# Kernel optimization log

Measured on AMD Instinct MI355X. Metric: run time of the kernel, lower is better.

## Reference

```python
import jax, jax.numpy as jnp
import numpy as np

N_NODES = 50000
N_EDGES = 600000
CLASSIC_DIM = 128
GRAPH_OUTPUT_DIM = 96
NUM_RELATIONS = 4


def setup_inputs() -> dict:
    key = jax.random.key(0)
    ks = jax.random.split(key, 10)
    x = jax.random.normal(ks[0], (N_NODES, CLASSIC_DIM), dtype=jnp.float32)
    edge_index = jax.random.randint(ks[1], (2, N_EDGES), 0, N_NODES, dtype=jnp.int64)
    edge_type = jax.random.randint(ks[2], (N_EDGES,), 0, NUM_RELATIONS, dtype=jnp.int64)
    s1 = 1.0 / np.sqrt(CLASSIC_DIM)
    W_root1 = jax.random.normal(ks[3], (CLASSIC_DIM, CLASSIC_DIM), dtype=jnp.float32) * s1
    W_rel1 = jax.random.normal(ks[4], (NUM_RELATIONS, CLASSIC_DIM, CLASSIC_DIM), dtype=jnp.float32) * s1
    b1 = jnp.zeros((CLASSIC_DIM,), dtype=jnp.float32)
    W_root2 = jax.random.normal(ks[5], (CLASSIC_DIM, GRAPH_OUTPUT_DIM), dtype=jnp.float32) * s1
    W_rel2 = jax.random.normal(ks[6], (NUM_RELATIONS, CLASSIC_DIM, GRAPH_OUTPUT_DIM), dtype=jnp.float32) * s1
    b2 = jnp.zeros((GRAPH_OUTPUT_DIM,), dtype=jnp.float32)
    return {"classic_features": x, "edge_index": edge_index, "edge_type": edge_type,
            "W_root1": W_root1, "W_rel1": W_rel1, "b1": b1,
            "W_root2": W_root2, "W_rel2": W_rel2, "b2": b2}


def _rgcn_layer(x, edge_index, edge_type, W_root, W_rel, b):
    # RGCN: h_i = W_root x_i + b + sum_r (1/deg_{i,r}) * W_r * sum_{j in N_r(i)} x_j
    # Aggregate-then-transform (valid by linearity) to keep the matmul small.
    src, dst = edge_index[0], edge_index[1]
    msgs = x[src]  # [E, d_in] irregular gather
    out = x @ W_root + b
    n = x.shape[0]
    num_rel = W_rel.shape[0]
    for r in range(num_rel):  # small fixed loop over relation types
        mask = (edge_type == r).astype(x.dtype)  # [E]
        agg = jax.ops.segment_sum(msgs * mask[:, None], dst, num_segments=n)  # [N, d_in]
        deg = jax.ops.segment_sum(mask, dst, num_segments=n)  # [N]
        agg = agg / jnp.maximum(deg, 1.0)[:, None]  # mean per relation (PyG default norm)
        out = out + agg @ W_rel[r]
    return out


def reference(classic_features, edge_index, edge_type, W_root1, W_rel1, b1, W_root2, W_rel2, b2):
    h = _rgcn_layer(classic_features, edge_index, edge_type, W_root1, W_rel1, b1)
    h = jax.nn.relu(h)
    # dropout(0.2) is identity in eval mode
    out = _rgcn_layer(h, edge_index, edge_type, W_root2, W_rel2, b2)
    return out
```

## Files before the change

kernel.cpp:

```cpp
#include <hip/hip_runtime.h>

#define DIM_IN 128
#define NREL 4
#define KTOT (DIM_IN + NREL * DIM_IN)
#define CAP 32

typedef __attribute__((ext_vector_type(8))) short short8;
typedef __attribute__((ext_vector_type(4))) float floatx4;

__device__ inline unsigned short f2bf(float f) {
    union { float f; unsigned int i; } c;
    c.f = f;
    unsigned int r = c.i + 0x7FFF + ((c.i >> 16) & 1);
    return (unsigned short)(r >> 16);
}
__device__ inline float bf2f(unsigned short u) {
    union { unsigned int i; float f; } c;
    c.i = ((unsigned int)u) << 16;
    return c.f;
}

__device__ inline void gload16_lds(const void* g, void* l) {
    __builtin_amdgcn_global_load_lds((const __attribute__((address_space(1))) unsigned int*)g,
                                     (__attribute__((address_space(3))) unsigned int*)l,
                                     16, 0, 0);
}

__global__ __launch_bounds__(256) void prep_kernel(
    const float* __restrict__ x, unsigned short* __restrict__ xb, int n4,
    const float* __restrict__ Wroot1, const float* __restrict__ Wrel1,
    unsigned short* __restrict__ Wt1,
    const float* __restrict__ Wroot2, const float* __restrict__ Wrel2,
    unsigned short* __restrict__ Wt2,
    const int* __restrict__ ei, const int* __restrict__ et,
    int* __restrict__ counts, unsigned short* __restrict__ bucket, int E) {
    int t = blockIdx.x * 256 + threadIdx.x;
    if (t < E) {
        int b = ei[E + t] * NREL + et[t];
        int slot = atomicAdd(&counts[b], 1);
        if (slot < CAP) bucket[(size_t)b * CAP + slot] = (unsigned short)ei[t];
    }
    if (t < n4) {
        float4 v = ((const float4*)x)[t];
        ushort4 o;
        o.x = f2bf(v.x); o.y = f2bf(v.y); o.z = f2bf(v.z); o.w = f2bf(v.w);
        ((ushort4*)xb)[t] = o;
    }
    if (t < 128 * KTOT) {
        int n = t / KTOT, k = t - n * KTOT;
        float v = (k < DIM_IN) ? Wroot1[(size_t)k * 128 + n]
                               : Wrel1[(size_t)(k - DIM_IN) * 128 + n];
        Wt1[t] = f2bf(v);
    }
    if (t < 96 * KTOT) {
        int n = t / KTOT, k = t - n * KTOT;
        float v = (k < DIM_IN) ? Wroot2[(size_t)k * 96 + n]
                               : Wrel2[(size_t)(k - DIM_IN) * 96 + n];
        Wt2[t] = f2bf(v);
    }
}

__global__ __launch_bounds__(256) void agg_kernel(
    const unsigned short* __restrict__ feat, const unsigned short* __restrict__ bucket,
    const int* __restrict__ counts, unsigned short* __restrict__ agg, int nb) {
    int l16 = threadIdx.x & 15;
    int g = (blockIdx.x * 256 + threadIdx.x) >> 4;
    if (g >= nb) return;
    int cnt = counts[g];
    int m = (cnt < CAP) ? cnt : CAP;
    const unsigned short* bk = bucket + (size_t)g * CAP;
    const unsigned short* fb = feat + l16 * 8;
    float acc[8];
#pragma unroll
    for (int j = 0; j < 8; j++) acc[j] = 0.f;
    for (int base = 0; base < m; base += 16) {
        int mm = m - base;
        if (mm > 16) mm = 16;
        int pick = (l16 < mm) ? l16 : (mm - 1);
        int idx = bk[base + pick];
        int s0 = __shfl(idx, 0, 16);
        short8 u = *(const short8*)(fb + (size_t)s0 * DIM_IN);
        for (int j = 1; j < mm; j++) {
            int sn = __shfl(idx, j, 16);
            short8 un = *(const short8*)(fb + (size_t)sn * DIM_IN);
#pragma unroll
            for (int c = 0; c < 8; c++) acc[c] += bf2f((unsigned short)u[c]);
            u = un;
        }
#pragma unroll
        for (int c = 0; c < 8; c++) acc[c] += bf2f((unsigned short)u[c]);
    }
    float sc = (cnt > 0) ? (1.0f / (float)cnt) : 0.f;
    short8 o;
#pragma unroll
    for (int j = 0; j < 8; j++) o[j] = (short)f2bf(acc[j] * sc);
    *(short8*)(agg + (size_t)g * DIM_IN + l16 * 8) = o;
}

template <int NOUT, bool STORE_BF16_RELU>
__global__ __launch_bounds__(256) void mfma_gemm_kernel(
    const unsigned short* __restrict__ xb,
    const unsigned short* __restrict__ agg,
    const unsigned short* __restrict__ Wt,
    const float* __restrict__ bias,
    void* __restrict__ outp,
    int N) {
    constexpr int NT = NOUT / 32;
    constexpr int APAN = 64 * 32;
    constexpr int BPAN = NOUT * 32;
    __shared__ unsigned short sA[2 * APAN];
    __shared__ unsigned short sB[2 * BPAN];
    const int t = threadIdx.x;
    const int w = t >> 6;
    const int lane = t & 63;
    const int q = lane >> 4;
    const int l15 = lane & 15;
    const int wm = w >> 1, wn = w & 1;
    const int m0 = blockIdx.x * 64;

    floatx4 acc[2][NT];
#pragma unroll
    for (int mt = 0; mt < 2; mt++)
#pragma unroll
        for (int nt = 0; nt < NT; nt++) acc[mt][nt] = (floatx4)0.f;

    for (int ks = 0; ks < KTOT / 64; ks++) {
        const int k0 = ks * 64;
#pragma unroll
        for (int r = 0; r < 2; r++) {
            int idx = t + r * 256;
            int panel = idx >> 8;
            int rem = idx & 255;
            int row = rem >> 2, ch = rem & 3;
            int rowg = m0 + row;
            if (rowg >= N) rowg = N - 1;
            int col = panel * 32 + ch * 8;
            const unsigned short* gp =
                (k0 < DIM_IN)
                    ? (xb + (size_t)rowg * DIM_IN + k0 + col)
                    : (agg + (size_t)rowg * (NREL * DIM_IN) + (k0 - DIM_IN) + col);
            gload16_lds(gp, sA + (size_t)idx * 8);
        }
#pragma unroll
        for (int r = 0; r < (NOUT * 8) / 256; r++) {
            int idx = t + r * 256;
            int panel = idx / (NOUT * 4);
            int rem = idx - panel * (NOUT * 4);
            int nrow = rem >> 2, ch = rem & 3;
            gload16_lds(Wt + (size_t)nrow * KTOT + k0 + panel * 32 + ch * 8,
                        sB + (size_t)idx * 8);
        }
        __syncthreads();
#pragma unroll
        for (int s = 0; s < 2; s++) {
            short8 aF[2], bF[NT];
#pragma unroll
            for (int mt = 0; mt < 2; mt++)
                aF[mt] = *(const short8*)(sA + s * APAN +
                                          (size_t)(wm * 32 + mt * 16 + l15) * 32 + q * 8);
#pragma unroll
            for (int nt = 0; nt < NT; nt++)
                bF[nt] = *(const short8*)(sB + s * BPAN +
                                          (size_t)(wn * (NOUT / 2) + nt * 16 + l15) * 32 + q * 8);
#pragma unroll
            for (int mt = 0; mt < 2; mt++)
#pragma unroll
                for (int nt = 0; nt < NT; nt++)
                    acc[mt][nt] = __builtin_amdgcn_mfma_f32_16x16x32_bf16(aF[mt], bF[nt],
                                                                          acc[mt][nt], 0, 0, 0);
        }
        __syncthreads();
    }

#pragma unroll
    for (int nt = 0; nt < NT; nt++) {
        int colg = wn * (NOUT / 2) + nt * 16 + l15;
        float bv = bias[colg];
#pragma unroll
        for (int mt = 0; mt < 2; mt++) {
            int rbase = m0 + wm * 32 + mt * 16 + q * 4;
#pragma unroll
            for (int r = 0; r < 4; r++) {
                int grow = rbase + r;
                if (grow < N) {
                    float v = acc[mt][nt][r] + bv;
                    if (STORE_BF16_RELU) {
                        v = fmaxf(v, 0.f);
                        ((unsigned short*)outp)[(size_t)grow * NOUT + colg] = f2bf(v);
                    } else {
                        ((float*)outp)[(size_t)grow * NOUT + colg] = v;
                    }
                }
            }
        }
    }
}

extern "C" void kernel_launch(void* const* d_in, const int* in_sizes, int n_in,
                              void* d_out, int out_size, void* d_ws, size_t ws_size,
                              hipStream_t stream) {
    const float* x = (const float*)d_in[0];
    const int* ei = (const int*)d_in[1];
    const int* et = (const int*)d_in[2];
    const float* Wroot1 = (const float*)d_in[3];
    const float* Wrel1 = (const float*)d_in[4];
    const float* b1 = (const float*)d_in[5];
    const float* Wroot2 = (const float*)d_in[6];
    const float* Wrel2 = (const float*)d_in[7];
    const float* b2 = (const float*)d_in[8];
    float* out = (float*)d_out;

    int N = in_sizes[0] / DIM_IN;
    int E = in_sizes[2];
    int nb = N * NREL;

    char* p = (char*)d_ws;
    unsigned short* xb = (unsigned short*)p;     p += (size_t)N * DIM_IN * 2;
    unsigned short* hb = (unsigned short*)p;     p += (size_t)N * DIM_IN * 2;
    unsigned short* agg = (unsigned short*)p;    p += (size_t)nb * DIM_IN * 2;
    unsigned short* Wt1 = (unsigned short*)p;    p += (size_t)128 * KTOT * 2;
    unsigned short* Wt2 = (unsigned short*)p;    p += (size_t)96 * KTOT * 2;
    int* counts = (int*)p;                       p += (size_t)nb * 4;
    unsigned short* bucket = (unsigned short*)p; p += (size_t)nb * CAP * 2;
    if ((size_t)(p - (char*)d_ws) > ws_size) return;

    int n4 = N * DIM_IN / 4;
    int prepWork = n4;
    if (prepWork < E) prepWork = E;
    if (prepWork < 128 * KTOT) prepWork = 128 * KTOT;

    hipMemsetAsync(counts, 0, (size_t)nb * sizeof(int), stream);
    prep_kernel<<<(prepWork + 255) / 256, 256, 0, stream>>>(
        x, xb, n4, Wroot1, Wrel1, Wt1, Wroot2, Wrel2, Wt2, ei, et, counts, bucket, E);

    int gAgg = (nb * 16 + 255) / 256;
    int gB = (N + 63) / 64;
    agg_kernel<<<gAgg, 256, 0, stream>>>(xb, bucket, counts, agg, nb);
    mfma_gemm_kernel<128, true><<<gB, 256, 0, stream>>>(xb, agg, Wt1, b1, hb, N);
    agg_kernel<<<gAgg, 256, 0, stream>>>(hb, bucket, counts, agg, nb);
    mfma_gemm_kernel<96, false><<<gB, 256, 0, stream>>>(hb, agg, Wt2, b2, out, N);
}
```

Baseline: 228.3 us.

## Fuse all stages into one persistent cooperative kernel with grid syncs

```diff
diff --git a/kernel.cpp b/kernel.cpp
--- a/kernel.cpp
+++ b/kernel.cpp
@@ -1,4 +1,7 @@
 #include <hip/hip_runtime.h>
+#include <hip/hip_cooperative_groups.h>
+
+namespace cg = cooperative_groups;
 
 #define DIM_IN 128
 #define NREL 4
@@ -26,15 +29,15 @@
                                      16, 0, 0);
 }
 
-__global__ __launch_bounds__(256) void prep_kernel(
-    const float* __restrict__ x, unsigned short* __restrict__ xb, int n4,
+
+__device__ __forceinline__ void prep_body(
+    int t, const float* __restrict__ x, unsigned short* __restrict__ xb, int n4,
     const float* __restrict__ Wroot1, const float* __restrict__ Wrel1,
     unsigned short* __restrict__ Wt1,
     const float* __restrict__ Wroot2, const float* __restrict__ Wrel2,
     unsigned short* __restrict__ Wt2,
     const int* __restrict__ ei, const int* __restrict__ et,
     int* __restrict__ counts, unsigned short* __restrict__ bucket, int E) {
-    int t = blockIdx.x * 256 + threadIdx.x;
     if (t < E) {
         int b = ei[E + t] * NREL + et[t];
         int slot = atomicAdd(&counts[b], 1);
@@ -60,12 +63,10 @@
     }
 }
 
-__global__ __launch_bounds__(256) void agg_kernel(
-    const unsigned short* __restrict__ feat, const unsigned short* __restrict__ bucket,
-    const int* __restrict__ counts, unsigned short* __restrict__ agg, int nb) {
-    int l16 = threadIdx.x & 15;
-    int g = (blockIdx.x * 256 + threadIdx.x) >> 4;
-    if (g >= nb) return;
+__device__ __forceinline__ void agg_body(
+    int g, int l16, const unsigned short* __restrict__ feat,
+    const unsigned short* __restrict__ bucket, const int* __restrict__ counts,
+    unsigned short* __restrict__ agg) {
     int cnt = counts[g];
     int m = (cnt < CAP) ? cnt : CAP;
     const unsigned short* bk = bucket + (size_t)g * CAP;
@@ -98,25 +99,19 @@
 }
 
 template <int NOUT, bool STORE_BF16_RELU>
-__global__ __launch_bounds__(256) void mfma_gemm_kernel(
-    const unsigned short* __restrict__ xb,
-    const unsigned short* __restrict__ agg,
-    const unsigned short* __restrict__ Wt,
-    const float* __restrict__ bias,
-    void* __restrict__ outp,
-    int N) {
+__device__ __forceinline__ void gemm_tile(
+    int m0, const unsigned short* __restrict__ xb, const unsigned short* __restrict__ agg,
+    const unsigned short* __restrict__ Wt, const float* __restrict__ bias,
+    void* __restrict__ outp, int N, unsigned short* sA, unsigned short* sB) {
     constexpr int NT = NOUT / 32;
     constexpr int APAN = 64 * 32;
     constexpr int BPAN = NOUT * 32;
-    __shared__ unsigned short sA[2 * APAN];
-    __shared__ unsigned short sB[2 * BPAN];
     const int t = threadIdx.x;
     const int w = t >> 6;
     const int lane = t & 63;
     const int q = lane >> 4;
     const int l15 = lane & 15;
     const int wm = w >> 1, wn = w & 1;
-    const int m0 = blockIdx.x * 64;
 
     floatx4 acc[2][NT];
 #pragma unroll
@@ -196,6 +191,82 @@
     }
 }
 
+
+__global__ __launch_bounds__(256) void prep_kernel(
+    const float* x, unsigned short* xb, int n4,
+    const float* Wroot1, const float* Wrel1, unsigned short* Wt1,
+    const float* Wroot2, const float* Wrel2, unsigned short* Wt2,
+    const int* ei, const int* et, int* counts, unsigned short* bucket, int E) {
+    int t = blockIdx.x * 256 + threadIdx.x;
+    prep_body(t, x, xb, n4, Wroot1, Wrel1, Wt1, Wroot2, Wrel2, Wt2, ei, et, counts, bucket, E);
+}
+
+__global__ __launch_bounds__(256) void agg_kernel(
+    const unsigned short* feat, const unsigned short* bucket,
+    const int* counts, unsigned short* agg, int nb) {
+    int l16 = threadIdx.x & 15;
+    int g = (blockIdx.x * 256 + threadIdx.x) >> 4;
+    if (g >= nb) return;
+    agg_body(g, l16, feat, bucket, counts, agg);
+}
+
+template <int NOUT, bool STORE_BF16_RELU>
+__global__ __launch_bounds__(256) void mfma_gemm_kernel(
+    const unsigned short* xb, const unsigned short* agg, const unsigned short* Wt,
+    const float* bias, void* outp, int N) {
+    __shared__ unsigned short sA[2 * 64 * 32];
+    __shared__ unsigned short sB[2 * NOUT * 32];
+    gemm_tile<NOUT, STORE_BF16_RELU>(blockIdx.x * 64, xb, agg, Wt, bias, outp, N, sA, sB);
+}
+
+__global__ __launch_bounds__(256, 4) void fused_all(
+    const float* x, unsigned short* xb, int n4,
+    const float* Wroot1, const float* Wrel1, unsigned short* Wt1,
+    const float* Wroot2, const float* Wrel2, unsigned short* Wt2,
+    const int* ei, const int* et, int* counts, unsigned short* bucket, int E,
+    unsigned short* aggbuf, unsigned short* hb,
+    const float* b1, const float* b2, float* out, int N, int prepWork) {
+    cg::grid_group grid = cg::this_grid();
+    __shared__ unsigned short sA[2 * 64 * 32];
+    __shared__ unsigned short sB[2 * 128 * 32];
+    const int nb = N * NREL;
+    const int tid = threadIdx.x;
+    const int gsz = gridDim.x;
+
+    for (int t = blockIdx.x * 256 + tid; t < prepWork; t += gsz * 256)
+        prep_body(t, x, xb, n4, Wroot1, Wrel1, Wt1, Wroot2, Wrel2, Wt2, ei, et, counts, bucket, E);
+    grid.sync();
+
+    {
+        int l16 = tid & 15;
+        int g0 = (blockIdx.x * 256 + tid) >> 4;
+        int gs = (gsz * 256) >> 4;
+        for (int g = g0; g < nb; g += gs) agg_body(g, l16, xb, bucket, counts, aggbuf);
+    }
+    grid.sync();
+
+    {
+        int gB = (N + 63) / 64;
+        for (int blk = blockIdx.x; blk < gB; blk += gsz)
+            gemm_tile<128, true>(blk * 64, xb, aggbuf, Wt1, b1, hb, N, sA, sB);
+    }
+    grid.sync();
+
+    {
+        int l16 = tid & 15;
+        int g0 = (blockIdx.x * 256 + tid) >> 4;
+        int gs = (gsz * 256) >> 4;
+        for (int g = g0; g < nb; g += gs) agg_body(g, l16, hb, bucket, counts, aggbuf);
+    }
+    grid.sync();
+
+    {
+        int gB = (N + 63) / 64;
+        for (int blk = blockIdx.x; blk < gB; blk += gsz)
+            gemm_tile<96, false>(blk * 64, hb, aggbuf, Wt2, b2, out, N, sA, sB);
+    }
+}
+
 extern "C" void kernel_launch(void* const* d_in, const int* in_sizes, int n_in,
                               void* d_out, int out_size, void* d_ws, size_t ws_size,
                               hipStream_t stream) {
@@ -230,11 +301,22 @@
     if (prepWork < 128 * KTOT) prepWork = 128 * KTOT;
 
     hipMemsetAsync(counts, 0, (size_t)nb * sizeof(int), stream);
+
+    void* args[] = {
+        (void*)&x, (void*)&xb, (void*)&n4,
+        (void*)&Wroot1, (void*)&Wrel1, (void*)&Wt1,
+        (void*)&Wroot2, (void*)&Wrel2, (void*)&Wt2,
+        (void*)&ei, (void*)&et, (void*)&counts, (void*)&bucket, (void*)&E,
+        (void*)&agg, (void*)&hb,
+        (void*)&b1, (void*)&b2, (void*)&out, (void*)&N, (void*)&prepWork};
+    hipError_t err = hipLaunchCooperativeKernel((const void*)fused_all, dim3(1024), dim3(256),
+                                                args, 0, stream);
+    if (err == hipSuccess) return;
+
+    int gAgg = (nb * 16 + 255) / 256;
+    int gB = (N + 63) / 64;
     prep_kernel<<<(prepWork + 255) / 256, 256, 0, stream>>>(
         x, xb, n4, Wroot1, Wrel1, Wt1, Wroot2, Wrel2, Wt2, ei, et, counts, bucket, E);
-
-    int gAgg = (nb * 16 + 255) / 256;
-    int gB = (N + 63) / 64;
     agg_kernel<<<gAgg, 256, 0, stream>>>(xb, bucket, counts, agg, nb);
     mfma_gemm_kernel<128, true><<<gB, 256, 0, stream>>>(xb, agg, Wt1, b1, hb, N);
     agg_kernel<<<gAgg, 256, 0, stream>>>(hb, bucket, counts, agg, nb);
```

Result: slower. 762.6 us (+234.0%).
